# Kernel optimization log

Hardware: AMD Instinct MI355X
Metric: run time of the kernel (lower is better)

Reference implementation:

```python
import jax, jax.numpy as jnp
import numpy as np

N_SRC = 50000
N_DST = 50000
N_EDGES = 800000
D_IN = 128
D_HID = 128
D_OUT = 128


def setup_inputs() -> dict:
    key = jax.random.key(0)
    ks = jax.random.split(key, 8)
    h_src = jax.random.normal(ks[0], (N_SRC, D_IN), dtype=jnp.float32)
    h_dst = jax.random.normal(ks[1], (N_DST, D_IN), dtype=jnp.float32)
    weights = jax.random.uniform(ks[2], (N_EDGES,), dtype=jnp.float32)
    edge_src = jax.random.randint(ks[3], (N_EDGES,), 0, N_SRC, dtype=jnp.int64)
    edge_dst = jax.random.randint(ks[4], (N_EDGES,), 0, N_DST, dtype=jnp.int64)
    # Xavier-uniform-ish init scaled like nn.init.xavier_uniform_(gain=sqrt(2))
    gain = float(np.sqrt(2.0))
    limQ = gain * float(np.sqrt(6.0 / (D_IN + D_HID)))
    limW = gain * float(np.sqrt(6.0 / (D_IN + D_HID + D_OUT)))
    Q_w = jax.random.uniform(ks[5], (D_HID, D_IN), minval=-limQ, maxval=limQ, dtype=jnp.float32)
    Q_b = jnp.zeros((D_HID,), dtype=jnp.float32)
    W_w = jax.random.uniform(ks[6], (D_OUT, D_IN + D_HID), minval=-limW, maxval=limW, dtype=jnp.float32)
    W_b = jnp.zeros((D_OUT,), dtype=jnp.float32)
    return {
        "h_src": h_src, "h_dst": h_dst, "weights": weights,
        "edge_src": edge_src, "edge_dst": edge_dst,
        "Q_w": Q_w, "Q_b": Q_b, "W_w": W_w, "W_b": W_b,
    }


def reference(h_src, h_dst, weights, edge_src, edge_dst, Q_w, Q_b, W_w, W_b):
    # n = relu(Q(h_src))  (dropout is identity in eval mode)
    n_src = jax.nn.relu(h_src @ Q_w.T + Q_b)                    # [N_src, H]
    w = weights.astype(jnp.float32)
    # u_mul_e + sum: weighted message aggregation per destination node
    msgs = n_src[edge_src] * w[:, None]                          # [E, H]
    n = jax.ops.segment_sum(msgs, edge_dst, num_segments=N_DST)  # [N_dst, H]
    # copy_e + sum: per-destination weight sum, clamped at 1
    ws = jax.ops.segment_sum(w, edge_dst, num_segments=N_DST)
    ws = jnp.clip(ws, 1.0, None)[:, None]                        # [N_dst, 1]
    z_in = jnp.concatenate([n / ws, h_dst], axis=1)              # [N_dst, H+D]
    z = jax.nn.relu(z_in @ W_w.T + W_b)                          # [N_dst, O]
    return z
```

## Files before the change

kernel.cpp:

```cpp
#include <hip/hip_runtime.h>
#include <hip/hip_bf16.h>

#define D 128
#define BSHIFT 7
#define BSIZE 128
#define NBUCK 391
#define CAP 3072
#define P1_EPB 4096
#define QPAD 136
#define WPAD 264

typedef __attribute__((ext_vector_type(8))) short bf16x8;
typedef __attribute__((ext_vector_type(4))) float floatx4;

__device__ __forceinline__ unsigned short f2bf(float f) {
    unsigned u = __float_as_uint(f);
    return (unsigned short)((u + 0x7FFFu + ((u >> 16) & 1u)) >> 16);
}
__device__ __forceinline__ float bf2f(unsigned short s) {
    return __uint_as_float(((unsigned)s) << 16);
}

__global__ __launch_bounds__(256)
void gemm1_mfma(const float* __restrict__ h, const float* __restrict__ Qw,
                const float* __restrict__ Qb, unsigned short* __restrict__ nsrc,
                int* __restrict__ gcursor, int M) {
    __shared__ unsigned short Bs[128 * QPAD];
    const int tid = threadIdx.x;
    const int lane = tid & 63;
    const int wv = tid >> 6;
    const int m0 = (blockIdx.x * 4 + wv) * 16;
    const int rquad = lane >> 4;
    const int rlow = lane & 15;
    const bool active = (m0 < M);

    if (blockIdx.x == 0) {
        for (int i = tid; i < NBUCK; i += 256) gcursor[i] = 0;
    }

    bf16x8 a[4];
    if (active) {
#pragma unroll
        for (int q = 0; q < 4; ++q) {
            const float* pa = h + (size_t)(m0 + rlow) * D + q * 32 + rquad * 8;
            float4 x = *(const float4*)pa;
            float4 y = *(const float4*)(pa + 4);
            bf16x8 t;
            t[0] = (short)f2bf(x.x); t[1] = (short)f2bf(x.y);
            t[2] = (short)f2bf(x.z); t[3] = (short)f2bf(x.w);
            t[4] = (short)f2bf(y.x); t[5] = (short)f2bf(y.y);
            t[6] = (short)f2bf(y.z); t[7] = (short)f2bf(y.w);
            a[q] = t;
        }
    }

#pragma unroll
    for (int c = tid; c < 4096; c += 256) {
        int row = c >> 5, col4 = (c & 31) * 4;
        float4 x = *(const float4*)(Qw + row * 128 + col4);
        ushort4 t;
        t.x = f2bf(x.x); t.y = f2bf(x.y); t.z = f2bf(x.z); t.w = f2bf(x.w);
        *(ushort4*)&Bs[row * QPAD + col4] = t;
    }
    __syncthreads();
    if (!active) return;

    floatx4 acc[8];
#pragma unroll
    for (int n = 0; n < 8; ++n) acc[n] = (floatx4)0.f;

#pragma unroll
    for (int n = 0; n < 8; ++n) {
#pragma unroll
        for (int q = 0; q < 4; ++q) {
            bf16x8 b = *(const bf16x8*)&Bs[(n * 16 + rlow) * QPAD + q * 32 + rquad * 8];
            acc[n] = __builtin_amdgcn_mfma_f32_16x16x32_bf16(a[q], b, acc[n], 0, 0, 0);
        }
    }

#pragma unroll
    for (int n = 0; n < 8; ++n) {
        int col = n * 16 + rlow;
        float bias = Qb[col];
#pragma unroll
        for (int r = 0; r < 4; ++r) {
            int row = m0 + rquad * 4 + r;
            nsrc[(size_t)row * D + col] = f2bf(fmaxf(acc[n][r] + bias, 0.f));
        }
    }
}

__global__ __launch_bounds__(256)
void pass1_bucket(const int* __restrict__ esrc, const int* __restrict__ edst,
                  const float* __restrict__ w, int* __restrict__ gcursor,
                  unsigned long long* __restrict__ staging, int E) {
    __shared__ int cnt[NBUCK];
    __shared__ int base[NBUCK];
    const int tid = threadIdx.x;
    const int e0 = blockIdx.x * P1_EPB;
    for (int i = tid; i < NBUCK; i += 256) cnt[i] = 0;
    __syncthreads();
#pragma unroll
    for (int i = 0; i < P1_EPB; i += 256) {
        int e = e0 + i + tid;
        if (e < E) atomicAdd(&cnt[edst[e] >> BSHIFT], 1);
    }
    __syncthreads();
    for (int i = tid; i < NBUCK; i += 256) {
        int c = cnt[i];
        base[i] = (c > 0) ? atomicAdd(&gcursor[i], c) : 0;
        cnt[i] = 0;
    }
    __syncthreads();
#pragma unroll
    for (int i = 0; i < P1_EPB; i += 256) {
        int e = e0 + i + tid;
        if (e < E) {
            int d = edst[e];
            int b = d >> BSHIFT;
            int pos = base[b] + atomicAdd(&cnt[b], 1);
            if (pos < CAP) {
                unsigned long long pk =
                    (unsigned long long)(unsigned)(esrc[e] | ((d & (BSIZE - 1)) << 16)) |
                    ((unsigned long long)__float_as_uint(w[e]) << 32);
                staging[(size_t)b * CAP + pos] = pk;
            }
        }
    }
}

__global__ __launch_bounds__(256)
void pass2_fill(const unsigned long long* __restrict__ staging,
                const int* __restrict__ gcursor,
                int2* __restrict__ offs2, unsigned long long* __restrict__ csr, int N) {
    __shared__ int cntA[BSIZE], sB[BSIZE];
    const int b = blockIdx.x;
    const int tid = threadIdx.x;
    int cnt = min(gcursor[b], CAP);
    const int base = b * CAP;
    const unsigned long long* st = staging + (size_t)b * CAP;

    if (tid < BSIZE) cntA[tid] = 0;
    __syncthreads();
    for (int i = tid; i < cnt; i += 256)
        atomicAdd(&cntA[(int)((st[i] >> 16) & (BSIZE - 1))], 1);
    __syncthreads();

    int v = (tid < BSIZE) ? cntA[tid] : 0;
    if (tid < BSIZE) sB[tid] = v;
    __syncthreads();
#pragma unroll
    for (int off = 1; off < BSIZE; off <<= 1) {
        int t = 0;
        if (tid < BSIZE && tid >= off) t = sB[tid - off];
        __syncthreads();
        if (tid < BSIZE) sB[tid] += t;
        __syncthreads();
    }
    int ex = (tid < BSIZE) ? (sB[tid] - v) : 0;
    if (tid < BSIZE) cntA[tid] = ex;
    __syncthreads();

    int node = b * BSIZE + tid;
    if (tid < BSIZE && node < N) offs2[node] = make_int2(base + ex, base + ex + v);

    for (int i = tid; i < cnt; i += 256) {
        unsigned long long pk = st[i];
        int dl = (int)((pk >> 16) & (BSIZE - 1));
        int slot = base + atomicAdd(&cntA[dl], 1);
        csr[slot] = (pk & 0xFFFFull) | (pk & 0xFFFFFFFF00000000ull);
    }
}

__global__ __launch_bounds__(256)
void gather(const unsigned long long* __restrict__ csr, const int2* __restrict__ offs2,
            const unsigned short* __restrict__ nsrc, unsigned short* __restrict__ nout, int N) {
    int node = __builtin_amdgcn_readfirstlane((int)((blockIdx.x * 256 + threadIdx.x) >> 6));
    int lane = threadIdx.x & 63;
    if (node >= N) return;
    int2 be = offs2[node];
    int beg = be.x, end = be.y;

    float a0 = 0.f, a1 = 0.f, a2 = 0.f, a3 = 0.f;
    float ws0 = 0.f, ws1 = 0.f;
    const int off2 = lane * 2;

    int i = beg;
    for (; i + 8 <= end; i += 8) {
        unsigned long long p[8];
        unsigned v[8];
        float wt[8];
#pragma unroll
        for (int j = 0; j < 8; ++j) p[j] = csr[i + j];
#pragma unroll
        for (int j = 0; j < 8; ++j) {
            wt[j] = __uint_as_float((unsigned)(p[j] >> 32));
            v[j] = *(const unsigned*)(nsrc + (size_t)(unsigned)p[j] * D + off2);
        }
#pragma unroll
        for (int j = 0; j < 8; j += 2) {
            a0 += bf2f((unsigned short)v[j]) * wt[j];
            a1 += bf2f((unsigned short)(v[j] >> 16)) * wt[j];
            a2 += bf2f((unsigned short)v[j + 1]) * wt[j + 1];
            a3 += bf2f((unsigned short)(v[j + 1] >> 16)) * wt[j + 1];
            ws0 += wt[j]; ws1 += wt[j + 1];
        }
    }
    for (; i + 4 <= end; i += 4) {
        unsigned long long p0 = csr[i + 0], p1 = csr[i + 1];
        unsigned long long p2 = csr[i + 2], p3 = csr[i + 3];
        float w0 = __uint_as_float((unsigned)(p0 >> 32));
        float w1 = __uint_as_float((unsigned)(p1 >> 32));
        float w2 = __uint_as_float((unsigned)(p2 >> 32));
        float w3 = __uint_as_float((unsigned)(p3 >> 32));
        unsigned v0 = *(const unsigned*)(nsrc + (size_t)(unsigned)p0 * D + off2);
        unsigned v1 = *(const unsigned*)(nsrc + (size_t)(unsigned)p1 * D + off2);
        unsigned v2 = *(const unsigned*)(nsrc + (size_t)(unsigned)p2 * D + off2);
        unsigned v3 = *(const unsigned*)(nsrc + (size_t)(unsigned)p3 * D + off2);
        a0 += bf2f((unsigned short)v0) * w0; a1 += bf2f((unsigned short)(v0 >> 16)) * w0;
        a2 += bf2f((unsigned short)v1) * w1; a3 += bf2f((unsigned short)(v1 >> 16)) * w1;
        a0 += bf2f((unsigned short)v2) * w2; a1 += bf2f((unsigned short)(v2 >> 16)) * w2;
        a2 += bf2f((unsigned short)v3) * w3; a3 += bf2f((unsigned short)(v3 >> 16)) * w3;
        ws0 += w0 + w2; ws1 += w1 + w3;
    }
    for (; i < end; ++i) {
        unsigned long long p = csr[i];
        float wt = __uint_as_float((unsigned)(p >> 32));
        unsigned v = *(const unsigned*)(nsrc + (size_t)(unsigned)p * D + off2);
        a0 += bf2f((unsigned short)v) * wt; a1 += bf2f((unsigned short)(v >> 16)) * wt;
        ws0 += wt;
    }

    float inv = 1.f / fmaxf(ws0 + ws1, 1.f);
    unsigned outv = (unsigned)f2bf((a0 + a2) * inv) | ((unsigned)f2bf((a1 + a3) * inv) << 16);
    *(unsigned*)(nout + (size_t)node * D + off2) = outv;
}

__global__ __launch_bounds__(256)
void gemm2_mfma(const unsigned short* __restrict__ nnorm, const float* __restrict__ hdst,
                const float* __restrict__ Ww, const float* __restrict__ Wb,
                float* __restrict__ out, int M) {
    __shared__ unsigned short Bs[128 * WPAD];
    const int tid = threadIdx.x;
    const int lane = tid & 63;
    const int wv = tid >> 6;
    const int m0 = (blockIdx.x * 4 + wv) * 16;
    const int rquad = lane >> 4;
    const int rlow = lane & 15;
    const bool active = (m0 < M);

    bf16x8 a[8];
    if (active) {
#pragma unroll
        for (int q = 0; q < 4; ++q)
            a[q] = *(const bf16x8*)(nnorm + (size_t)(m0 + rlow) * D + q * 32 + rquad * 8);
#pragma unroll
        for (int q = 4; q < 8; ++q) {
            const float* pa = hdst + (size_t)(m0 + rlow) * D + (q - 4) * 32 + rquad * 8;
            float4 x = *(const float4*)pa;
            float4 y = *(const float4*)(pa + 4);
            bf16x8 t;
            t[0] = (short)f2bf(x.x); t[1] = (short)f2bf(x.y);
            t[2] = (short)f2bf(x.z); t[3] = (short)f2bf(x.w);
            t[4] = (short)f2bf(y.x); t[5] = (short)f2bf(y.y);
            t[6] = (short)f2bf(y.z); t[7] = (short)f2bf(y.w);
            a[q] = t;
        }
    }

#pragma unroll
    for (int c = tid; c < 8192; c += 256) {
        int row = c >> 6, col4 = (c & 63) * 4;
        float4 x = *(const float4*)(Ww + row * 256 + col4);
        ushort4 t;
        t.x = f2bf(x.x); t.y = f2bf(x.y); t.z = f2bf(x.z); t.w = f2bf(x.w);
        *(ushort4*)&Bs[row * WPAD + col4] = t;
    }
    __syncthreads();
    if (!active) return;

    floatx4 acc[8];
#pragma unroll
    for (int n = 0; n < 8; ++n) acc[n] = (floatx4)0.f;

#pragma unroll
    for (int n = 0; n < 8; ++n) {
#pragma unroll
        for (int q = 0; q < 8; ++q) {
            bf16x8 b = *(const bf16x8*)&Bs[(n * 16 + rlow) * WPAD + q * 32 + rquad * 8];
            acc[n] = __builtin_amdgcn_mfma_f32_16x16x32_bf16(a[q], b, acc[n], 0, 0, 0);
        }
    }

#pragma unroll
    for (int n = 0; n < 8; ++n) {
        int col = n * 16 + rlow;
        float bias = Wb[col];
#pragma unroll
        for (int r = 0; r < 4; ++r) {
            int row = m0 + rquad * 4 + r;
            out[(size_t)row * D + col] = fmaxf(acc[n][r] + bias, 0.f);
        }
    }
}

extern "C" void kernel_launch(void* const* d_in, const int* in_sizes, int n_in,
                              void* d_out, int out_size, void* d_ws, size_t ws_size,
                              hipStream_t stream) {
    const float* h_src   = (const float*)d_in[0];
    const float* h_dst   = (const float*)d_in[1];
    const float* weights = (const float*)d_in[2];
    const int*   esrc    = (const int*)d_in[3];
    const int*   edst    = (const int*)d_in[4];
    const float* Q_w     = (const float*)d_in[5];
    const float* Q_b     = (const float*)d_in[6];
    const float* W_w     = (const float*)d_in[7];
    const float* W_b     = (const float*)d_in[8];

    const int N_SRC = in_sizes[0] / D;
    const int N_DST = in_sizes[1] / D;
    const int E     = in_sizes[2];

    char* ws = (char*)d_ws;
    int*  gcursor = (int*)(ws + 0);
    int2* offs2   = (int2*)(ws + 4096);
    unsigned long long* staging = (unsigned long long*)(ws + 409600);
    unsigned long long* csr     = (unsigned long long*)(ws + 409600 + (size_t)NBUCK * CAP * 8);
    unsigned short* nsrc16  = (unsigned short*)(ws + 409600 + 2 * (size_t)NBUCK * CAP * 8);
    unsigned short* nnorm16 = (unsigned short*)(ws + 409600 + 2 * (size_t)NBUCK * CAP * 8
                                                + (size_t)N_SRC * D * 2);

    float* out = (float*)d_out;

    gemm1_mfma<<<(N_SRC + 63) / 64, 256, 0, stream>>>(h_src, Q_w, Q_b, nsrc16, gcursor, N_SRC);

    pass1_bucket<<<(E + P1_EPB - 1) / P1_EPB, 256, 0, stream>>>(esrc, edst, weights,
                                                                gcursor, staging, E);

    pass2_fill<<<NBUCK, 256, 0, stream>>>(staging, gcursor, offs2, csr, N_DST);

    gather<<<(N_DST * 64 + 255) / 256, 256, 0, stream>>>(csr, offs2, nsrc16, nnorm16, N_DST);

    gemm2_mfma<<<(N_DST + 63) / 64, 256, 0, stream>>>(nnorm16, h_dst, W_w, W_b, out, N_DST);
}
```

Before: 195.7 us.

## Fuse source GEMM and edge bucketing into one heterogeneous launch

Merges the first GEMM kernel and the pass-1 edge bucketing kernel into a single launch. Blocks below G1B run the GEMM and the rest run the bucketing, so the two independent stages overlap on the GPU and one launch boundary goes away. The gcursor reset moves from block 0 of the GEMM to a hipMemsetAsync, because bucketing blocks now run concurrently and could otherwise race with the reset. The memset adds a small stream operation, and the bucketing blocks now carry the GEMM's larger shared-memory allocation, which may lower their occupancy.

New measurement: 191.1 us. 1.02x faster.

```diff
diff --git a/kernel.cpp b/kernel.cpp
--- a/kernel.cpp
+++ b/kernel.cpp
@@ -22,108 +22,103 @@
 }
 
 __global__ __launch_bounds__(256)
-void gemm1_mfma(const float* __restrict__ h, const float* __restrict__ Qw,
-                const float* __restrict__ Qb, unsigned short* __restrict__ nsrc,
-                int* __restrict__ gcursor, int M) {
+void fused_g1_p1(const float* __restrict__ h, const float* __restrict__ Qw,
+                 const float* __restrict__ Qb, unsigned short* __restrict__ nsrc, int M,
+                 const int* __restrict__ esrc, const int* __restrict__ edst,
+                 const float* __restrict__ w, int* __restrict__ gcursor,
+                 unsigned long long* __restrict__ staging, int E, int G1B) {
     __shared__ unsigned short Bs[128 * QPAD];
     const int tid = threadIdx.x;
-    const int lane = tid & 63;
-    const int wv = tid >> 6;
-    const int m0 = (blockIdx.x * 4 + wv) * 16;
-    const int rquad = lane >> 4;
-    const int rlow = lane & 15;
-    const bool active = (m0 < M);
-
-    if (blockIdx.x == 0) {
-        for (int i = tid; i < NBUCK; i += 256) gcursor[i] = 0;
-    }
-
-    bf16x8 a[4];
-    if (active) {
-#pragma unroll
-        for (int q = 0; q < 4; ++q) {
-            const float* pa = h + (size_t)(m0 + rlow) * D + q * 32 + rquad * 8;
-            float4 x = *(const float4*)pa;
-            float4 y = *(const float4*)(pa + 4);
-            bf16x8 t;
-            t[0] = (short)f2bf(x.x); t[1] = (short)f2bf(x.y);
-            t[2] = (short)f2bf(x.z); t[3] = (short)f2bf(x.w);
-            t[4] = (short)f2bf(y.x); t[5] = (short)f2bf(y.y);
-            t[6] = (short)f2bf(y.z); t[7] = (short)f2bf(y.w);
-            a[q] = t;
-        }
-    }
-
-#pragma unroll
-    for (int c = tid; c < 4096; c += 256) {
-        int row = c >> 5, col4 = (c & 31) * 4;
-        float4 x = *(const float4*)(Qw + row * 128 + col4);
-        ushort4 t;
-        t.x = f2bf(x.x); t.y = f2bf(x.y); t.z = f2bf(x.z); t.w = f2bf(x.w);
-        *(ushort4*)&Bs[row * QPAD + col4] = t;
-    }
-    __syncthreads();
-    if (!active) return;
-
-    floatx4 acc[8];
-#pragma unroll
-    for (int n = 0; n < 8; ++n) acc[n] = (floatx4)0.f;
-
-#pragma unroll
-    for (int n = 0; n < 8; ++n) {
-#pragma unroll
-        for (int q = 0; q < 4; ++q) {
-            bf16x8 b = *(const bf16x8*)&Bs[(n * 16 + rlow) * QPAD + q * 32 + rquad * 8];
-            acc[n] = __builtin_amdgcn_mfma_f32_16x16x32_bf16(a[q], b, acc[n], 0, 0, 0);
-        }
-    }
-
-#pragma unroll
-    for (int n = 0; n < 8; ++n) {
-        int col = n * 16 + rlow;
-        float bias = Qb[col];
-#pragma unroll
-        for (int r = 0; r < 4; ++r) {
-            int row = m0 + rquad * 4 + r;
-            nsrc[(size_t)row * D + col] = f2bf(fmaxf(acc[n][r] + bias, 0.f));
-        }
-    }
-}
-
-__global__ __launch_bounds__(256)
-void pass1_bucket(const int* __restrict__ esrc, const int* __restrict__ edst,
-                  const float* __restrict__ w, int* __restrict__ gcursor,
-                  unsigned long long* __restrict__ staging, int E) {
-    __shared__ int cnt[NBUCK];
-    __shared__ int base[NBUCK];
-    const int tid = threadIdx.x;
-    const int e0 = blockIdx.x * P1_EPB;
-    for (int i = tid; i < NBUCK; i += 256) cnt[i] = 0;
-    __syncthreads();
-#pragma unroll
-    for (int i = 0; i < P1_EPB; i += 256) {
-        int e = e0 + i + tid;
-        if (e < E) atomicAdd(&cnt[edst[e] >> BSHIFT], 1);
-    }
-    __syncthreads();
-    for (int i = tid; i < NBUCK; i += 256) {
-        int c = cnt[i];
-        base[i] = (c > 0) ? atomicAdd(&gcursor[i], c) : 0;
-        cnt[i] = 0;
-    }
-    __syncthreads();
-#pragma unroll
-    for (int i = 0; i < P1_EPB; i += 256) {
-        int e = e0 + i + tid;
-        if (e < E) {
-            int d = edst[e];
-            int b = d >> BSHIFT;
-            int pos = base[b] + atomicAdd(&cnt[b], 1);
-            if (pos < CAP) {
-                unsigned long long pk =
-                    (unsigned long long)(unsigned)(esrc[e] | ((d & (BSIZE - 1)) << 16)) |
-                    ((unsigned long long)__float_as_uint(w[e]) << 32);
-                staging[(size_t)b * CAP + pos] = pk;
+
+    if ((int)blockIdx.x < G1B) {
+        const int lane = tid & 63;
+        const int wv = tid >> 6;
+        const int m0 = (blockIdx.x * 4 + wv) * 16;
+        const int rquad = lane >> 4;
+        const int rlow = lane & 15;
+        const bool active = (m0 < M);
+
+        bf16x8 a[4];
+        if (active) {
+#pragma unroll
+            for (int q = 0; q < 4; ++q) {
+                const float* pa = h + (size_t)(m0 + rlow) * D + q * 32 + rquad * 8;
+                float4 x = *(const float4*)pa;
+                float4 y = *(const float4*)(pa + 4);
+                bf16x8 t;
+                t[0] = (short)f2bf(x.x); t[1] = (short)f2bf(x.y);
+                t[2] = (short)f2bf(x.z); t[3] = (short)f2bf(x.w);
+                t[4] = (short)f2bf(y.x); t[5] = (short)f2bf(y.y);
+                t[6] = (short)f2bf(y.z); t[7] = (short)f2bf(y.w);
+                a[q] = t;
+            }
+        }
+
+#pragma unroll
+        for (int c = tid; c < 4096; c += 256) {
+            int row = c >> 5, col4 = (c & 31) * 4;
+            float4 x = *(const float4*)(Qw + row * 128 + col4);
+            ushort4 t;
+            t.x = f2bf(x.x); t.y = f2bf(x.y); t.z = f2bf(x.z); t.w = f2bf(x.w);
+            *(ushort4*)&Bs[row * QPAD + col4] = t;
+        }
+        __syncthreads();
+        if (!active) return;
+
+        floatx4 acc[8];
+#pragma unroll
+        for (int n = 0; n < 8; ++n) acc[n] = (floatx4)0.f;
+
+#pragma unroll
+        for (int n = 0; n < 8; ++n) {
+#pragma unroll
+            for (int q = 0; q < 4; ++q) {
+                bf16x8 b = *(const bf16x8*)&Bs[(n * 16 + rlow) * QPAD + q * 32 + rquad * 8];
+                acc[n] = __builtin_amdgcn_mfma_f32_16x16x32_bf16(a[q], b, acc[n], 0, 0, 0);
+            }
+        }
+
+#pragma unroll
+        for (int n = 0; n < 8; ++n) {
+            int col = n * 16 + rlow;
+            float bias = Qb[col];
+#pragma unroll
+            for (int r = 0; r < 4; ++r) {
+                int row = m0 + rquad * 4 + r;
+                nsrc[(size_t)row * D + col] = f2bf(fmaxf(acc[n][r] + bias, 0.f));
+            }
+        }
+    } else {
+        int* cnt  = (int*)Bs;
+        int* base = cnt + NBUCK;
+        const int e0 = ((int)blockIdx.x - G1B) * P1_EPB;
+        for (int i = tid; i < NBUCK; i += 256) cnt[i] = 0;
+        __syncthreads();
+#pragma unroll
+        for (int i = 0; i < P1_EPB; i += 256) {
+            int e = e0 + i + tid;
+            if (e < E) atomicAdd(&cnt[edst[e] >> BSHIFT], 1);
+        }
+        __syncthreads();
+        for (int i = tid; i < NBUCK; i += 256) {
+            int c = cnt[i];
+            base[i] = (c > 0) ? atomicAdd(&gcursor[i], c) : 0;
+            cnt[i] = 0;
+        }
+        __syncthreads();
+#pragma unroll
+        for (int i = 0; i < P1_EPB; i += 256) {
+            int e = e0 + i + tid;
+            if (e < E) {
+                int d = edst[e];
+                int b = d >> BSHIFT;
+                int pos = base[b] + atomicAdd(&cnt[b], 1);
+                if (pos < CAP) {
+                    unsigned long long pk =
+                        (unsigned long long)(unsigned)(esrc[e] | ((d & (BSIZE - 1)) << 16)) |
+                        ((unsigned long long)__float_as_uint(w[e]) << 32);
+                    staging[(size_t)b * CAP + pos] = pk;
+                }
             }
         }
     }
@@ -332,10 +327,13 @@
 
     float* out = (float*)d_out;
 
-    gemm1_mfma<<<(N_SRC + 63) / 64, 256, 0, stream>>>(h_src, Q_w, Q_b, nsrc16, gcursor, N_SRC);
-
-    pass1_bucket<<<(E + P1_EPB - 1) / P1_EPB, 256, 0, stream>>>(esrc, edst, weights,
-                                                                gcursor, staging, E);
+    const int G1B = (N_SRC + 63) / 64;
+    const int P1B = (E + P1_EPB - 1) / P1_EPB;
+
+    hipMemsetAsync(gcursor, 0, NBUCK * sizeof(int), stream);
+
+    fused_g1_p1<<<G1B + P1B, 256, 0, stream>>>(h_src, Q_w, Q_b, nsrc16, N_SRC,
+                                               esrc, edst, weights, gcursor, staging, E, G1B);
 
     pass2_fill<<<NBUCK, 256, 0, stream>>>(staging, gcursor, offs2, csr, N_DST);
 
```
